# Kernel tuning notes

Measured on AMD Instinct MI355X. Metric: run time of the kernel, lower is better.

## Reference

```python
import jax, jax.numpy as jnp
import numpy as np

C = 512
QK = C // 8  # 64
B, L = 8, 4096


def setup_inputs() -> dict:
    key = jax.random.key(0)
    ks = jax.random.split(key, 8)
    s = 0.02
    return {
        "x": jax.random.normal(ks[0], (B, C, L), dtype=jnp.float32),
        "Wq": jax.random.normal(ks[1], (QK, C), dtype=jnp.float32) * s,
        "bq": jax.random.normal(ks[2], (QK,), dtype=jnp.float32) * s,
        "Wk": jax.random.normal(ks[3], (QK, C), dtype=jnp.float32) * s,
        "bk": jax.random.normal(ks[4], (QK,), dtype=jnp.float32) * s,
        "Wv": jax.random.normal(ks[5], (C, C), dtype=jnp.float32) * s,
        "bv": jax.random.normal(ks[6], (C,), dtype=jnp.float32) * s,
        "gamma": jax.random.normal(ks[7], (1,), dtype=jnp.float32) * 0.1,
    }


def reference(x, Wq, bq, Wk, bk, Wv, bv, gamma):
    # 1x1 convs are per-position linear projections over channels
    q = jnp.einsum('bcl,dc->bld', x, Wq) + bq            # [B, L, QK]  (proj_query, permuted)
    k = jnp.einsum('bcl,dc->bdl', x, Wk) + bk[:, None]   # [B, QK, L]  (proj_key)
    v = jnp.einsum('bcl,dc->bdl', x, Wv) + bv[:, None]   # [B, C, L]   (proj_value)
    energy = jnp.einsum('bid,bdj->bij', q, k)            # [B, L, L]
    attn = jax.nn.softmax(energy, axis=-1)               # softmax over j
    out = jnp.einsum('bcj,bij->bci', v, attn)            # [B, C, L]
    return gamma * out + x
```

## Files before the change

kernel.cpp:

```cpp
#include <hip/hip_runtime.h>
#include <math.h>

#define BB 8
#define CC 512
#define LL 4096
#define DQK 64

typedef short short8 __attribute__((ext_vector_type(8)));
typedef unsigned short ushort4v __attribute__((ext_vector_type(4)));
typedef unsigned short ushort8v __attribute__((ext_vector_type(8)));
typedef float floatx4 __attribute__((ext_vector_type(4)));
typedef unsigned int uint4v __attribute__((ext_vector_type(4)));

__device__ __forceinline__ unsigned short f2bf(float f) {
    union { float f; unsigned u; } v; v.f = f;
    unsigned r = v.u + 0x7fffu + ((v.u >> 16) & 1u);
    return (unsigned short)(r >> 16);
}

__device__ __forceinline__ void load_lds16(const void* gptr, void* lptr) {
    __builtin_amdgcn_global_load_lds(
        (const __attribute__((address_space(1))) unsigned int*)gptr,
        (__attribute__((address_space(3))) unsigned int*)lptr, 16, 0, 0);
}

__device__ __forceinline__ unsigned cvt_pk_bf16(float lo, float hi) {
    unsigned r;
    asm("v_cvt_pk_bf16_f32 %0, %1, %2" : "=v"(r) : "v"(lo), "v"(hi));
    return r;
}

__global__ __launch_bounds__(256) void k_transpose(const float* __restrict__ x,
                                                   unsigned short* __restrict__ xt) {
    __shared__ unsigned short tile[64][72];
    int l0 = blockIdx.x * 64, c0 = blockIdx.y * 64, b = blockIdx.z;
    int t = threadIdx.x;
    int r  = t >> 2;
    int ch = (t & 3) * 16;
    const float* src = x + ((size_t)b * CC + c0 + r) * LL + l0 + ch;
#pragma unroll
    for (int j = 0; j < 4; ++j) {
        floatx4 v = *(const floatx4*)(src + j * 4);
        ushort4v u = { f2bf(v[0]), f2bf(v[1]), f2bf(v[2]), f2bf(v[3]) };
        *(ushort4v*)(&tile[r][ch + j * 4]) = u;
    }
    __syncthreads();
    int lr  = t >> 2;
    int cch = (t & 3) * 16;
    ushort8v o0, o1;
#pragma unroll
    for (int j = 0; j < 8; ++j) o0[j] = tile[cch + j][lr];
#pragma unroll
    for (int j = 0; j < 8; ++j) o1[j] = tile[cch + 8 + j][lr];
    unsigned short* dst = xt + ((size_t)b * LL + l0 + lr) * CC + c0 + cch;
    *(ushort8v*)(dst)     = o0;
    *(ushort8v*)(dst + 8) = o1;
}

__global__ void k_castw(const float* __restrict__ wq, const float* __restrict__ wk,
                        const float* __restrict__ wv,
                        unsigned short* __restrict__ wqb, unsigned short* __restrict__ wkb,
                        unsigned short* __restrict__ wvb) {
    int i = blockIdx.x * 256 + threadIdx.x;
    if (i < DQK * CC) { wqb[i] = f2bf(wq[i]); wkb[i] = f2bf(wk[i]); }
    wvb[i] = f2bf(wv[i]);
}

__global__ __launch_bounds__(256) void k_projall(const unsigned short* __restrict__ xt,
                                                 const unsigned short* __restrict__ wqb,
                                                 const unsigned short* __restrict__ wkb,
                                                 const unsigned short* __restrict__ wvb,
                                                 const float* __restrict__ bq,
                                                 const float* __restrict__ bk,
                                                 const float* __restrict__ bv,
                                                 unsigned short* __restrict__ qout,
                                                 unsigned short* __restrict__ kout,
                                                 unsigned short* __restrict__ vout) {
    int l0 = blockIdx.x * 64;
    int b  = blockIdx.y;
    int tid = threadIdx.x;
    int w = tid >> 6, lane = tid & 63;
    int lane16 = lane & 15, g = lane >> 4;
    __shared__ unsigned short xtile[64 * 512];
    {
        const unsigned short* xg = xt + ((size_t)b * LL + l0) * CC;
        int pg = tid & 63;
#pragma unroll
        for (int ci = 0; ci < 16; ++ci) {
            int r  = ci * 4 + (tid >> 6);
            int sg = (pg & 56) | ((pg ^ r) & 7);
            load_lds16(xg + (size_t)r * CC + sg * 8, xtile + ((size_t)ci * 256 + tid) * 8);
        }
    }

    int xe = (g ^ (lane16 & 7)) * 8;
    int xo = ((g + 4) ^ (lane16 & 7)) * 8;

    auto loadW = [&](short8 (&af)[16], int z) {
        const unsigned short* base;
        if (z < 8)       base = wvb + (size_t)(z * 64 + w * 16 + lane16) * CC;
        else if (z == 8) base = wqb + (size_t)(w * 16 + lane16) * CC;
        else             base = wkb + (size_t)(w * 16 + lane16) * CC;
        base += g * 8;
#pragma unroll
        for (int kk = 0; kk < 16; ++kk) af[kk] = *(const short8*)(base + kk * 32);
    };

    auto comp = [&](short8 (&af)[16], int z) {
#pragma unroll
        for (int nt = 0; nt < 4; ++nt) {
            floatx4 acc = {0.f, 0.f, 0.f, 0.f};
#pragma unroll
            for (int kk = 0; kk < 16; ++kk) {
                int off = (nt * 16 + lane16) * 512 + (kk >> 1) * 64 + ((kk & 1) ? xo : xe);
                short8 bfrag = *(const short8*)(xtile + off);
                acc = __builtin_amdgcn_mfma_f32_16x16x32_bf16(af[kk], bfrag, acc, 0, 0, 0);
            }
            int l = l0 + nt * 16 + lane16;
            if (z < 8) {
#pragma unroll
                for (int r = 0; r < 4; ++r) {
                    int d = z * 64 + w * 16 + g * 4 + r;
                    vout[((size_t)b * CC + d) * LL + l] = f2bf(acc[r] + bv[d]);
                }
            } else {
                const float* bias = (z == 8) ? bq : bk;
                float sc = (z == 8) ? 1.4426950408889634f : 1.0f;
                ushort4v o;
#pragma unroll
                for (int r = 0; r < 4; ++r)
                    o[r] = f2bf((acc[r] + bias[w * 16 + g * 4 + r]) * sc);
                unsigned short* dst = ((z == 8) ? qout : kout)
                                      + ((size_t)b * LL + l) * DQK + w * 16 + g * 4;
                *(ushort4v*)dst = o;
            }
        }
    };

    short8 afA[16], afB[16];
    loadW(afA, 0);
    __syncthreads();

    for (int z = 0; z < 10; z += 2) {
        loadW(afB, z + 1);
        comp(afA, z);
        if (z + 2 < 10) loadW(afA, z + 2);
        comp(afB, z + 1);
    }
}

__global__ __launch_bounds__(256, 2) void k_attn(const unsigned short* __restrict__ q,
                                                 const unsigned short* __restrict__ kws,
                                                 const unsigned short* __restrict__ vws,
                                                 const float* __restrict__ x,
                                                 const float* __restrict__ gamma,
                                                 float* __restrict__ out) {
    int bid = blockIdx.x + 32 * blockIdx.y + 256 * blockIdx.z;
    int x8  = bid & 7;
    int ii  = bid >> 3;
    int wg  = (x8 + 8 * (ii >> 5)) * 32 + (ii & 31);
    int i0 = (wg & 31) * 128;
    int b  = (wg >> 5) & 7;
    int c0 = (wg >> 8) * 256;

    int tid = threadIdx.x;
    int w = tid >> 6, lane = tid & 63;
    int lane16 = lane & 15, g = lane >> 4;
    int iw = i0 + w * 32;

    __shared__ unsigned short kt[2][64 * 64];
    __shared__ unsigned short vt[2][256 * 64];

    short8 qf[2][2];
#pragma unroll
    for (int m = 0; m < 2; ++m) {
        const unsigned short* qrow = q + ((size_t)b * LL + iw + m * 16 + lane16) * DQK + g * 8;
        qf[m][0] = *(const short8*)(qrow);
        qf[m][1] = *(const short8*)(qrow + 32);
    }

    const unsigned short* kglob = kws + (size_t)b * LL * DQK;
    const unsigned short* vglob = vws + ((size_t)b * CC + c0) * LL;
    int gr    = (tid & 7) ^ ((tid >> 3) & 7);
    int koff0 = (tid >> 3) * DQK + gr * 8;
    int voff0 = (tid >> 3) * LL  + gr * 8;

    int kro[2], vro[2];
#pragma unroll
    for (int kk = 0; kk < 2; ++kk) {
        int sw = (kk * 4 + g) ^ (lane16 & 7);
        kro[kk] = lane16 * 64 + sw * 8;
        vro[kk] = lane16 * 64 + sw * 8;
    }

    short8 ones;
#pragma unroll
    for (int j = 0; j < 8; ++j) ones[j] = (short)0x3f80;

    floatx4 O[2][16];
#pragma unroll
    for (int m = 0; m < 2; ++m)
#pragma unroll
        for (int nt = 0; nt < 16; ++nt) O[m][nt] = {0.f, 0.f, 0.f, 0.f};
    floatx4 Ol[2];
#pragma unroll
    for (int m = 0; m < 2; ++m) Ol[m] = {0.f, 0.f, 0.f, 0.f};

    auto stage = [&](int j0n, int buf) {
        const unsigned short* ks = kglob + j0n * DQK + koff0;
        unsigned short* kd = &kt[buf][tid * 8];
        load_lds16(ks, kd);
        load_lds16(ks + 2048, kd + 2048);
        const unsigned short* vs = vglob + j0n + voff0;
        unsigned short* vd = &vt[buf][tid * 8];
#pragma unroll
        for (int i = 0; i < 8; ++i)
            load_lds16(vs + i * 131072, vd + i * 2048);
    };

    auto softmax_half = [&](floatx4 (&Sh)[2][2], short8 (&paD)[2]) {
#pragma unroll
        for (int m = 0; m < 2; ++m) {
            float e0[4], e1[4];
#pragma unroll
            for (int r = 0; r < 4; ++r) {
                e0[r] = __builtin_amdgcn_exp2f(Sh[m][0][r]);
                e1[r] = __builtin_amdgcn_exp2f(Sh[m][1][r]);
            }
            unsigned A0 = cvt_pk_bf16(e0[0], e0[1]);
            unsigned A1 = cvt_pk_bf16(e0[2], e0[3]);
            unsigned B0 = cvt_pk_bf16(e1[0], e1[1]);
            unsigned B1 = cvt_pk_bf16(e1[2], e1[3]);
            asm("v_permlane32_swap_b32 %0, %1" : "+v"(A0), "+v"(B0));
            asm("v_permlane16_swap_b32 %0, %1" : "+v"(A0), "+v"(B0));
            asm("v_permlane32_swap_b32 %0, %1" : "+v"(A1), "+v"(B1));
            asm("v_permlane16_swap_b32 %0, %1" : "+v"(A1), "+v"(B1));
            uint4v pw = { A0, A1, B0, B1 };
            paD[m] = *(short8*)&pw;
            Ol[m] = __builtin_amdgcn_mfma_f32_16x16x32_bf16(paD[m], ones, Ol[m], 0, 0, 0);
        }
    };

    stage(0, 0);
    int cur = 0;
    for (int j0 = 0; j0 < LL; j0 += 64) {
        __syncthreads();
        if (j0 + 64 < LL) stage(j0 + 64, cur ^ 1);

        const unsigned short* kbp = kt[cur];
        const unsigned short* vbp = vt[cur];

        floatx4 Sa[2][2], Sb[2][2];
#pragma unroll
        for (int m = 0; m < 2; ++m)
#pragma unroll
            for (int nt = 0; nt < 2; ++nt) { Sa[m][nt] = {0.f,0.f,0.f,0.f}; Sb[m][nt] = {0.f,0.f,0.f,0.f}; }

        short8 ka0 = *(const short8*)(kbp + kro[0]);
        short8 ka1 = *(const short8*)(kbp + kro[1]);
        short8 kb0 = *(const short8*)(kbp + kro[0] + 1024);
        short8 kb1 = *(const short8*)(kbp + kro[1] + 1024);
#pragma unroll
        for (int m = 0; m < 2; ++m) {
            Sa[m][0] = __builtin_amdgcn_mfma_f32_16x16x32_bf16(ka0, qf[m][0], Sa[m][0], 0, 0, 0);
            Sa[m][0] = __builtin_amdgcn_mfma_f32_16x16x32_bf16(ka1, qf[m][1], Sa[m][0], 0, 0, 0);
            Sa[m][1] = __builtin_amdgcn_mfma_f32_16x16x32_bf16(kb0, qf[m][0], Sa[m][1], 0, 0, 0);
            Sa[m][1] = __builtin_amdgcn_mfma_f32_16x16x32_bf16(kb1, qf[m][1], Sa[m][1], 0, 0, 0);
        }
        short8 kc0 = *(const short8*)(kbp + kro[0] + 2048);
        short8 kc1 = *(const short8*)(kbp + kro[1] + 2048);
        short8 kd0 = *(const short8*)(kbp + kro[0] + 3072);
        short8 kd1 = *(const short8*)(kbp + kro[1] + 3072);
#pragma unroll
        for (int m = 0; m < 2; ++m) {
            Sb[m][0] = __builtin_amdgcn_mfma_f32_16x16x32_bf16(kc0, qf[m][0], Sb[m][0], 0, 0, 0);
            Sb[m][0] = __builtin_amdgcn_mfma_f32_16x16x32_bf16(kc1, qf[m][1], Sb[m][0], 0, 0, 0);
            Sb[m][1] = __builtin_amdgcn_mfma_f32_16x16x32_bf16(kd0, qf[m][0], Sb[m][1], 0, 0, 0);
            Sb[m][1] = __builtin_amdgcn_mfma_f32_16x16x32_bf16(kd1, qf[m][1], Sb[m][1], 0, 0, 0);
        }

        short8 pa0[2], pa1[2];
        softmax_half(Sa, pa0);

        __builtin_amdgcn_s_setprio(1);
#pragma unroll
        for (int nt = 0; nt < 8; ++nt) {
            short8 vf = *(const short8*)(vbp + vro[0] + nt * 1024);
#pragma unroll
            for (int m = 0; m < 2; ++m)
                O[m][nt] = __builtin_amdgcn_mfma_f32_16x16x32_bf16(pa0[m], vf, O[m][nt], 0, 0, 0);
        }
        __builtin_amdgcn_s_setprio(0);

        softmax_half(Sb, pa1);

        __builtin_amdgcn_s_setprio(1);
#pragma unroll
        for (int nt = 8; nt < 16; ++nt) {
            short8 vf = *(const short8*)(vbp + vro[0] + nt * 1024);
#pragma unroll
            for (int m = 0; m < 2; ++m)
                O[m][nt] = __builtin_amdgcn_mfma_f32_16x16x32_bf16(pa0[m], vf, O[m][nt], 0, 0, 0);
        }
#pragma unroll
        for (int nt = 0; nt < 16; ++nt) {
            short8 vf = *(const short8*)(vbp + vro[1] + nt * 1024);
#pragma unroll
            for (int m = 0; m < 2; ++m)
                O[m][nt] = __builtin_amdgcn_mfma_f32_16x16x32_bf16(pa1[m], vf, O[m][nt], 0, 0, 0);
        }
        __builtin_amdgcn_s_setprio(0);
        cur ^= 1;
    }

    float linv[2][4];
#pragma unroll
    for (int m = 0; m < 2; ++m)
#pragma unroll
        for (int r = 0; r < 4; ++r) linv[m][r] = 1.f / Ol[m][r];

    float gam = gamma[0];
#pragma unroll
    for (int m = 0; m < 2; ++m)
#pragma unroll
        for (int nt = 0; nt < 16; ++nt) {
            int c = c0 + nt * 16 + lane16;
            size_t base = ((size_t)b * CC + c) * LL + iw + m * 16 + g * 4;
            floatx4 xv = *(const floatx4*)(x + base);
            floatx4 o;
#pragma unroll
            for (int r = 0; r < 4; ++r) o[r] = gam * (O[m][nt][r] * linv[m][r]) + xv[r];
            *(floatx4*)(out + base) = o;
        }
}

extern "C" void kernel_launch(void* const* d_in, const int* in_sizes, int n_in,
                              void* d_out, int out_size, void* d_ws, size_t ws_size,
                              hipStream_t stream) {
    const float* x     = (const float*)d_in[0];
    const float* Wq    = (const float*)d_in[1];
    const float* bq    = (const float*)d_in[2];
    const float* Wk    = (const float*)d_in[3];
    const float* bk    = (const float*)d_in[4];
    const float* Wv    = (const float*)d_in[5];
    const float* bv    = (const float*)d_in[6];
    const float* gamma = (const float*)d_in[7];
    float* out = (float*)d_out;

    unsigned short* xt  = (unsigned short*)d_ws;
    unsigned short* qb  = xt  + (size_t)BB * LL * CC;
    unsigned short* kb  = qb  + (size_t)BB * LL * DQK;
    unsigned short* vb  = kb  + (size_t)BB * LL * DQK;
    unsigned short* wqb = vb  + (size_t)BB * CC * LL;
    unsigned short* wkb = wqb + (size_t)DQK * CC;
    unsigned short* wvb = wkb + (size_t)DQK * CC;

    k_transpose<<<dim3(LL / 64, CC / 64, BB), 256, 0, stream>>>(x, xt);
    k_castw<<<dim3((CC * CC) / 256), 256, 0, stream>>>(Wq, Wk, Wv, wqb, wkb, wvb);
    k_projall<<<dim3(LL / 64, BB), 256, 0, stream>>>(xt, wqb, wkb, wvb, bq, bk, bv, qb, kb, vb);
    k_attn<<<dim3(LL / 128, BB, CC / 256), 256, 0, stream>>>(qb, kb, vb, x, gamma, out);
}
```

Before: 356.5 us.

## Split K/V staging waits in attention and halve projection weight register buffers

In the attention kernel, the full __syncthreads at each tile is replaced by explicit vmcnt waits plus barriers. The loop first waits only for the K tile, so the QK MFMAs and the first softmax half can run while the V tile's global-to-LDS loads are still in flight. A second wait and barrier sits before the PV products. In the projection kernel, weights are now double-buffered in half-K chunks of 8 fragments instead of 16, with four accumulators live, which cuts register pressure and spreads the weight-load latency. The risk is that the hard-coded vmcnt counts assume exactly 10 async loads per stage and are fragile if the staging changes.

```diff
diff --git a/kernel.cpp b/kernel.cpp
--- a/kernel.cpp
+++ b/kernel.cpp
@@ -96,32 +96,52 @@
     int xe = (g ^ (lane16 & 7)) * 8;
     int xo = ((g + 4) ^ (lane16 & 7)) * 8;
 
-    auto loadW = [&](short8 (&af)[16], int z) {
+    auto loadW8 = [&](short8 (&af)[8], int hs) {
+        int z = hs >> 1, kh = hs & 1;
         const unsigned short* base;
         if (z < 8)       base = wvb + (size_t)(z * 64 + w * 16 + lane16) * CC;
         else if (z == 8) base = wqb + (size_t)(w * 16 + lane16) * CC;
         else             base = wkb + (size_t)(w * 16 + lane16) * CC;
-        base += g * 8;
-#pragma unroll
-        for (int kk = 0; kk < 16; ++kk) af[kk] = *(const short8*)(base + kk * 32);
+        base += g * 8 + kh * 256;
+#pragma unroll
+        for (int kk = 0; kk < 8; ++kk) af[kk] = *(const short8*)(base + kk * 32);
     };
 
-    auto comp = [&](short8 (&af)[16], int z) {
-#pragma unroll
-        for (int nt = 0; nt < 4; ++nt) {
-            floatx4 acc = {0.f, 0.f, 0.f, 0.f};
-#pragma unroll
-            for (int kk = 0; kk < 16; ++kk) {
+    short8 wA[8], wB[8];
+    loadW8(wA, 0);
+    __syncthreads();
+
+    for (int z = 0; z < 10; ++z) {
+        loadW8(wB, z * 2 + 1);
+        floatx4 acc[4];
+#pragma unroll
+        for (int nt = 0; nt < 4; ++nt) acc[nt] = {0.f, 0.f, 0.f, 0.f};
+#pragma unroll
+        for (int nt = 0; nt < 4; ++nt)
+#pragma unroll
+            for (int kk = 0; kk < 8; ++kk) {
                 int off = (nt * 16 + lane16) * 512 + (kk >> 1) * 64 + ((kk & 1) ? xo : xe);
                 short8 bfrag = *(const short8*)(xtile + off);
-                acc = __builtin_amdgcn_mfma_f32_16x16x32_bf16(af[kk], bfrag, acc, 0, 0, 0);
+                acc[nt] = __builtin_amdgcn_mfma_f32_16x16x32_bf16(wA[kk], bfrag, acc[nt], 0, 0, 0);
             }
+        if (z + 1 < 10) loadW8(wA, (z + 1) * 2);
+#pragma unroll
+        for (int nt = 0; nt < 4; ++nt)
+#pragma unroll
+            for (int kk = 0; kk < 8; ++kk) {
+                int kk8 = kk + 8;
+                int off = (nt * 16 + lane16) * 512 + (kk8 >> 1) * 64 + ((kk8 & 1) ? xo : xe);
+                short8 bfrag = *(const short8*)(xtile + off);
+                acc[nt] = __builtin_amdgcn_mfma_f32_16x16x32_bf16(wB[kk], bfrag, acc[nt], 0, 0, 0);
+            }
+#pragma unroll
+        for (int nt = 0; nt < 4; ++nt) {
             int l = l0 + nt * 16 + lane16;
             if (z < 8) {
 #pragma unroll
                 for (int r = 0; r < 4; ++r) {
                     int d = z * 64 + w * 16 + g * 4 + r;
-                    vout[((size_t)b * CC + d) * LL + l] = f2bf(acc[r] + bv[d]);
+                    vout[((size_t)b * CC + d) * LL + l] = f2bf(acc[nt][r] + bv[d]);
                 }
             } else {
                 const float* bias = (z == 8) ? bq : bk;
@@ -129,23 +149,12 @@
                 ushort4v o;
 #pragma unroll
                 for (int r = 0; r < 4; ++r)
-                    o[r] = f2bf((acc[r] + bias[w * 16 + g * 4 + r]) * sc);
+                    o[r] = f2bf((acc[nt][r] + bias[w * 16 + g * 4 + r]) * sc);
                 unsigned short* dst = ((z == 8) ? qout : kout)
                                       + ((size_t)b * LL + l) * DQK + w * 16 + g * 4;
                 *(ushort4v*)dst = o;
             }
         }
-    };
-
-    short8 afA[16], afB[16];
-    loadW(afA, 0);
-    __syncthreads();
-
-    for (int z = 0; z < 10; z += 2) {
-        loadW(afB, z + 1);
-        comp(afA, z);
-        if (z + 2 < 10) loadW(afA, z + 2);
-        comp(afB, z + 1);
     }
 }
 
@@ -206,11 +215,13 @@
 #pragma unroll
     for (int m = 0; m < 2; ++m) Ol[m] = {0.f, 0.f, 0.f, 0.f};
 
-    auto stage = [&](int j0n, int buf) {
+    auto stageK = [&](int j0n, int buf) {
         const unsigned short* ks = kglob + j0n * DQK + koff0;
         unsigned short* kd = &kt[buf][tid * 8];
-        load_lds16(ks, kd);
+        load_lds16(ks,        kd);
         load_lds16(ks + 2048, kd + 2048);
+    };
+    auto stageV = [&](int j0n, int buf) {
         const unsigned short* vs = vglob + j0n + voff0;
         unsigned short* vd = &vt[buf][tid * 8];
 #pragma unroll
@@ -241,11 +252,15 @@
         }
     };
 
-    stage(0, 0);
+    stageK(0, 0);
+    stageV(0, 0);
     int cur = 0;
     for (int j0 = 0; j0 < LL; j0 += 64) {
-        __syncthreads();
-        if (j0 + 64 < LL) stage(j0 + 64, cur ^ 1);
+        bool more = (j0 + 64 < LL);
+
+        asm volatile("s_waitcnt vmcnt(8)" ::: "memory");
+        __builtin_amdgcn_s_barrier();
+        if (more) { stageK(j0 + 64, cur ^ 1); stageV(j0 + 64, cur ^ 1); }
 
         const unsigned short* kbp = kt[cur];
         const unsigned short* vbp = vt[cur];
@@ -281,6 +296,10 @@
 
         short8 pa0[2], pa1[2];
         softmax_half(Sa, pa0);
+
+        if (more) asm volatile("s_waitcnt vmcnt(10)" ::: "memory");
+        else      asm volatile("s_waitcnt vmcnt(0)"  ::: "memory");
+        __builtin_amdgcn_s_barrier();
 
         __builtin_amdgcn_s_setprio(1);
 #pragma unroll
```

New measurement: 359.3 us. No clear change (+0.8%).
